# Kernel optimization log

Measured on AMD Instinct MI355X. Metric: run time of the kernel, lower is better.

The kernel has to match this reference:

```python
import jax, jax.numpy as jnp
import numpy as np

IN_DIM = 768
OUT_DIM = 768
NUM = IN_DIM * OUT_DIM
NUM_F = 8


def setup_inputs() -> dict:
    key = jax.random.key(0)
    k1, k2, k3 = jax.random.split(key, 3)
    x = jax.random.normal(k1, (32, 12, 64), dtype=jnp.float32)
    grid = jnp.arange(NUM_F, dtype=jnp.float32) + 1.0  # torch: arange(num_f)+1
    coef = jax.random.uniform(k2, (NUM, NUM_F), dtype=jnp.float32)
    bias_w = jax.random.normal(k3, (1, OUT_DIM), dtype=jnp.float32)
    scale_base = jnp.ones((NUM,), dtype=jnp.float32)
    scale_sp = jnp.ones((NUM,), dtype=jnp.float32)
    return {"x": x, "grid": grid, "coef": coef, "bias_w": bias_w,
            "scale_base": scale_base, "scale_sp": scale_sp}


def reference(x, grid, coef, bias_w, scale_base, scale_sp):
    batch = x.shape[0]
    out_dim = bias_w.shape[1]
    num = coef.shape[0]
    in_dim = num // out_dim
    # flatten [B, C, F] -> [B, in_dim]
    x2 = x.reshape(batch, in_dim)
    # broadcast each input feature to every output: [B, out_dim, in_dim] -> [num, B]
    xr = jnp.broadcast_to(x2[:, None, :], (batch, out_dim, in_dim)).reshape(batch, num).T
    base = jax.nn.silu(xr)                                  # [num, B]
    # sin basis: [num, num_f, B]
    f = jnp.sin(grid[None, :, None] * xr[:, None, :])
    f_out = jnp.einsum('ij,ijk->ik', coef, f)               # [num, B]
    f_out = (scale_sp[:, None] * f_out + scale_base[:, None] * base).T  # [B, num]
    y = f_out.reshape(batch, out_dim, in_dim).sum(axis=2)   # [B, out_dim]
    return y + bias_w
```

## Files before the change

### kernel.cpp

```cpp
#include <hip/hip_runtime.h>
#include <math.h>

#define IN_DIM 768
#define OUT_DIM 768
#define BATCH 32
#define NUM_F 8
#define SPAD 12

#define O_TILE 16
#define I_SPLIT 16
#define I_CHUNK (IN_DIM / I_SPLIT)

__global__ __launch_bounds__(256) void build_S(const float* __restrict__ x,
                                               const float* __restrict__ grid,
                                               const float* __restrict__ bias_w,
                                               float* __restrict__ S,
                                               float* __restrict__ y) {
    int idx = blockIdx.x * 256 + threadIdx.x;
    if (idx >= BATCH * IN_DIM) return;
    float xv = x[idx];
    float* out = S + (size_t)idx * SPAD;
    float4 a, b4;
    a.x  = __sinf(grid[0] * xv);
    a.y  = __sinf(grid[1] * xv);
    a.z  = __sinf(grid[2] * xv);
    a.w  = __sinf(grid[3] * xv);
    b4.x = __sinf(grid[4] * xv);
    b4.y = __sinf(grid[5] * xv);
    b4.z = __sinf(grid[6] * xv);
    b4.w = __sinf(grid[7] * xv);
    *(float4*)(out)     = a;
    *(float4*)(out + 4) = b4;
    out[8] = xv / (1.0f + __expf(-xv));
    y[idx] = bias_w[idx % OUT_DIM];
}

__global__ __launch_bounds__(256) void fused_reduce(const float* __restrict__ S,
                                                    const float* __restrict__ coef,
                                                    const float* __restrict__ scale_base,
                                                    const float* __restrict__ scale_sp,
                                                    float* __restrict__ y) {
    __shared__ float red[8 * 512];
    const int t  = threadIdx.x;
    const int b  = t & 31;
    const int g  = t >> 5;
    const int ob = blockIdx.x / I_SPLIT;
    const int is = blockIdx.x % I_SPLIT;
    const int o0 = ob * O_TILE;
    const int i0 = is * I_CHUNK;

    float acc[O_TILE];
#pragma unroll
    for (int ol = 0; ol < O_TILE; ++ol) acc[ol] = 0.0f;

    for (int i = i0 + g; i < i0 + I_CHUNK; i += 8) {
        const float4* sp = (const float4*)(S + (size_t)(b * IN_DIM + i) * SPAD);
        const float4 sA = sp[0];
        const float4 sB = sp[1];
        const float  s8 = S[(size_t)(b * IN_DIM + i) * SPAD + 8];
#pragma unroll
        for (int ol = 0; ol < O_TILE; ++ol) {
            const int n = (o0 + ol) * IN_DIM + i;
            const float4* cp = (const float4*)(coef + (size_t)n * 8);
            const float4 c0 = cp[0];
            const float4 c1 = cp[1];
            const float ssp = scale_sp[n];
            const float sb  = scale_base[n];
            float dot = c0.x * sA.x + c0.y * sA.y + c0.z * sA.z + c0.w * sA.w
                      + c1.x * sB.x + c1.y * sB.y + c1.z * sB.z + c1.w * sB.w;
            acc[ol] += ssp * dot + sb * s8;
        }
    }

#pragma unroll
    for (int ol = 0; ol < O_TILE; ++ol)
        red[g * 512 + b * O_TILE + ol] = acc[ol];
    __syncthreads();

#pragma unroll
    for (int rep = 0; rep < 2; ++rep) {
        const int idx2 = t + rep * 256;
        const int b2  = idx2 >> 4;
        const int ol2 = idx2 & 15;
        float sum = 0.0f;
#pragma unroll
        for (int g2 = 0; g2 < 8; ++g2) sum += red[g2 * 512 + idx2];
        atomicAdd(&y[b2 * OUT_DIM + o0 + ol2], sum);
    }
}

extern "C" void kernel_launch(void* const* d_in, const int* in_sizes, int n_in,
                              void* d_out, int out_size, void* d_ws, size_t ws_size,
                              hipStream_t stream) {
    const float* x          = (const float*)d_in[0];
    const float* grid       = (const float*)d_in[1];
    const float* coef       = (const float*)d_in[2];
    const float* bias_w     = (const float*)d_in[3];
    const float* scale_base = (const float*)d_in[4];
    const float* scale_sp   = (const float*)d_in[5];
    float* y = (float*)d_out;
    float* S = (float*)d_ws;

    build_S<<<(BATCH * IN_DIM + 255) / 256, 256, 0, stream>>>(x, grid, bias_w, S, y);
    fused_reduce<<<(OUT_DIM / O_TILE) * I_SPLIT, 256, 0, stream>>>(S, coef, scale_base,
                                                                   scale_sp, y);
}
```

Measured before the change: 105.2 us.

## Fuse sin/silu basis computation into the reduction kernel and drop the S workspace

Removes the intermediate S buffer: each thread now computes the sin and silu basis for its 4 contiguous input features directly from x in registers, instead of reading a precomputed S. The first kernel now only seeds y with the bias. I_SPLIT goes from 16 to 24, so each of the 8 thread groups handles exactly 4 consecutive inputs, which allows float4 loads of scale_sp and scale_base and contiguous coef reads. The aim is to cut the S write and read traffic and to improve coef streaming. In exchange, the sin evaluations are repeated across every output-tile block, more registers are used (launch bounds of 4 blocks), and there are more atomics.

```diff
diff --git a/kernel.cpp b/kernel.cpp
--- a/kernel.cpp
+++ b/kernel.cpp
@@ -4,42 +4,23 @@
 #define IN_DIM 768
 #define OUT_DIM 768
 #define BATCH 32
-#define NUM_F 8
-#define SPAD 12
 
 #define O_TILE 16
-#define I_SPLIT 16
+#define I_SPLIT 24
 #define I_CHUNK (IN_DIM / I_SPLIT)
 
-__global__ __launch_bounds__(256) void build_S(const float* __restrict__ x,
-                                               const float* __restrict__ grid,
-                                               const float* __restrict__ bias_w,
-                                               float* __restrict__ S,
-                                               float* __restrict__ y) {
+__global__ __launch_bounds__(256) void seed_y(const float* __restrict__ bias_w,
+                                              float* __restrict__ y) {
     int idx = blockIdx.x * 256 + threadIdx.x;
-    if (idx >= BATCH * IN_DIM) return;
-    float xv = x[idx];
-    float* out = S + (size_t)idx * SPAD;
-    float4 a, b4;
-    a.x  = __sinf(grid[0] * xv);
-    a.y  = __sinf(grid[1] * xv);
-    a.z  = __sinf(grid[2] * xv);
-    a.w  = __sinf(grid[3] * xv);
-    b4.x = __sinf(grid[4] * xv);
-    b4.y = __sinf(grid[5] * xv);
-    b4.z = __sinf(grid[6] * xv);
-    b4.w = __sinf(grid[7] * xv);
-    *(float4*)(out)     = a;
-    *(float4*)(out + 4) = b4;
-    out[8] = xv / (1.0f + __expf(-xv));
-    y[idx] = bias_w[idx % OUT_DIM];
+    if (idx < BATCH * OUT_DIM) y[idx] = bias_w[idx % OUT_DIM];
 }
 
-__global__ __launch_bounds__(256) void fused_reduce(const float* __restrict__ S,
-                                                    const float* __restrict__ coef,
-                                                    const float* __restrict__ scale_base,
-                                                    const float* __restrict__ scale_sp,
-                                                    float* __restrict__ y) {
+__global__ __launch_bounds__(256, 4) void slayer_fused(const float* __restrict__ x,
+                                                       const float* __restrict__ grid,
+                                                       const float* __restrict__ coef,
+                                                       const float* __restrict__ scale_base,
+                                                       const float* __restrict__ scale_sp,
+                                                       float* __restrict__ y) {
     __shared__ float red[8 * 512];
     const int t  = threadIdx.x;
     const int b  = t & 31;
@@ -47,28 +28,48 @@
     const int ob = blockIdx.x / I_SPLIT;
     const int is = blockIdx.x % I_SPLIT;
     const int o0 = ob * O_TILE;
-    const int i0 = is * I_CHUNK;
+    const int i0 = is * I_CHUNK + g * 4;
+
+    float gr[8];
+#pragma unroll
+    for (int j = 0; j < 8; ++j) gr[j] = grid[j];
+
+    const float4 xv = *(const float4*)(x + b * IN_DIM + i0);
+    const float xq[4] = {xv.x, xv.y, xv.z, xv.w};
+
+    float sn[4][8];
+    float si[4];
+#pragma unroll
+    for (int q = 0; q < 4; ++q) {
+#pragma unroll
+        for (int j = 0; j < 8; ++j) sn[q][j] = __sinf(gr[j] * xq[q]);
+        si[q] = xq[q] / (1.0f + __expf(-xq[q]));
+    }
+
+    const float* cbase = coef + ((size_t)(o0 * IN_DIM + i0)) * 8;
+    const float* spb   = scale_sp + o0 * IN_DIM + i0;
+    const float* sbb   = scale_base + o0 * IN_DIM + i0;
 
     float acc[O_TILE];
 #pragma unroll
     for (int ol = 0; ol < O_TILE; ++ol) acc[ol] = 0.0f;
 
-    for (int i = i0 + g; i < i0 + I_CHUNK; i += 8) {
-        const float4* sp = (const float4*)(S + (size_t)(b * IN_DIM + i) * SPAD);
-        const float4 sA = sp[0];
-        const float4 sB = sp[1];
-        const float  s8 = S[(size_t)(b * IN_DIM + i) * SPAD + 8];
 #pragma unroll
-        for (int ol = 0; ol < O_TILE; ++ol) {
-            const int n = (o0 + ol) * IN_DIM + i;
-            const float4* cp = (const float4*)(coef + (size_t)n * 8);
-            const float4 c0 = cp[0];
-            const float4 c1 = cp[1];
-            const float ssp = scale_sp[n];
-            const float sb  = scale_base[n];
-            float dot = c0.x * sA.x + c0.y * sA.y + c0.z * sA.z + c0.w * sA.w
-                      + c1.x * sB.x + c1.y * sB.y + c1.z * sB.z + c1.w * sB.w;
-            acc[ol] += ssp * dot + sb * s8;
+    for (int ol = 0; ol < O_TILE; ++ol) {
+        const float* c = cbase + (size_t)ol * (IN_DIM * 8);
+        const float4 sp4 = *(const float4*)(spb + ol * IN_DIM);
+        const float4 sb4 = *(const float4*)(sbb + ol * IN_DIM);
+        const float spq[4] = {sp4.x, sp4.y, sp4.z, sp4.w};
+        const float sbq[4] = {sb4.x, sb4.y, sb4.z, sb4.w};
+#pragma unroll
+        for (int q = 0; q < 4; ++q) {
+            const float4 c0 = *(const float4*)(c + q * 8);
+            const float4 c1 = *(const float4*)(c + q * 8 + 4);
+            float dot = c0.x * sn[q][0] + c0.y * sn[q][1]
+                      + c0.z * sn[q][2] + c0.w * sn[q][3]
+                      + c1.x * sn[q][4] + c1.y * sn[q][5]
+                      + c1.z * sn[q][6] + c1.w * sn[q][7];
+            acc[ol] += spq[q] * dot + sbq[q] * si[q];
         }
     }
 
@@ -99,9 +100,8 @@
     const float* scale_base = (const float*)d_in[4];
     const float* scale_sp   = (const float*)d_in[5];
     float* y = (float*)d_out;
-    float* S = (float*)d_ws;
 
-    build_S<<<(BATCH * IN_DIM + 255) / 256, 256, 0, stream>>>(x, grid, bias_w, S, y);
-    fused_reduce<<<(OUT_DIM / O_TILE) * I_SPLIT, 256, 0, stream>>>(S, coef, scale_base,
-                                                                   scale_sp, y);
+    seed_y<<<(BATCH * OUT_DIM + 255) / 256, 256, 0, stream>>>(bias_w, y);
+    slayer_fused<<<(OUT_DIM / O_TILE) * I_SPLIT, 256, 0, stream>>>(x, grid, coef,
+                                                                   scale_base, scale_sp, y);
 }
```

After: 106.3 us. About the same (+1.1%).
